# Kernel tuning notes

Hardware: AMD Instinct MI355X
Metric: run time of the kernel (lower is better)

## Reference

```python
import jax, jax.numpy as jnp
import numpy as np

N = 100000   # nodes
E = 1600000  # edges
IN = 32      # in_dim
D = 64       # embed_dim
G = 128      # num graphs
EPS = 1e-5   # BatchNorm eps


def setup_inputs() -> dict:
    key = jax.random.key(0)
    ks = jax.random.split(key, 12)
    s_in = 1.0 / np.sqrt(IN)
    s_d = 1.0 / np.sqrt(D)
    return {
        "x": jax.random.normal(ks[0], (N, IN), jnp.float32),
        "edge_index": jax.random.randint(ks[1], (2, E), 0, N),
        "batch": jnp.sort(jax.random.randint(ks[2], (N,), 0, G)),
        "W_embed": jax.random.normal(ks[3], (IN, D), jnp.float32) * s_in,
        "W1": jax.random.normal(ks[4], (D, D), jnp.float32) * s_d,
        "b1": jnp.zeros((D,), jnp.float32),
        "g1": jnp.ones((D,), jnp.float32),
        "bt1": jnp.zeros((D,), jnp.float32),
        "W2": jax.random.normal(ks[5], (D, D), jnp.float32) * s_d,
        "b2": jnp.zeros((D,), jnp.float32),
        "g2": jnp.ones((D,), jnp.float32),
        "bt2": jnp.zeros((D,), jnp.float32),
    }


def reference(x, edge_index, batch, W_embed, W1, b1, g1, bt1, W2, b2, g2, bt2):
    src, dst = edge_index[0], edge_index[1]
    # GCN symmetric norm with self loops: deg = in-degree + 1 (self loop)
    deg = jnp.zeros((N,), x.dtype).at[dst].add(1.0) + 1.0
    dis = jax.lax.rsqrt(deg)                      # deg^{-1/2}, [N]
    enorm = dis[src] * dis[dst]                   # per-edge norm, [E]
    self_norm = dis * dis                         # self-loop norm, [N]

    def gcn_bn(h, W, b, g, bt, relu):
        hw = h @ W                                # linear first (GCNConv)
        msg = hw[src] * enorm[:, None]            # [E, D] gather + scale
        agg = jax.ops.segment_sum(msg, dst, num_segments=N)
        agg = agg + hw * self_norm[:, None] + b   # self loops + bias
        # BatchNorm1d (training mode: batch stats, biased var)
        mu = agg.mean(axis=0)
        var = agg.var(axis=0)
        hn = (agg - mu) * jax.lax.rsqrt(var + EPS) * g + bt
        return jnp.maximum(hn, 0.0) if relu else hn

    h = x @ W_embed                               # node_embed (Linear, no bias)
    h = gcn_bn(h, W1, b1, g1, bt1, relu=True)     # ReLU only between layers
    h = gcn_bn(h, W2, b2, g2, bt2, relu=False)
    h_pool = jax.ops.segment_sum(h, batch, num_segments=G)  # global_add_pool
    return (h, h_pool)
```

## Files before the change

kernel.cpp:

```cpp
#include <hip/hip_runtime.h>

#define NN 100000
#define NE 1600000
#define IN_DIM 32
#define DD 64
#define NG 128
#define BN_EPS 1e-5f
#define AGG_BLOCKS 2048

typedef unsigned short ushort_t;
typedef unsigned int uint_t;

__device__ __forceinline__ ushort_t f2bf(float f) {
    uint_t u = __float_as_uint(f);
    u = (u + 0x7FFFu + ((u >> 16) & 1u)) >> 16;
    return (ushort_t)u;
}
__device__ __forceinline__ uint_t pack2(float a, float b) {
    return (uint_t)f2bf(a) | ((uint_t)f2bf(b) << 16);
}
__device__ __forceinline__ float bflo(uint_t u) { return __uint_as_float(u << 16); }
__device__ __forceinline__ float bfhi(uint_t u) { return __uint_as_float(u & 0xFFFF0000u); }

__global__ void init_k(int* __restrict__ ints, long n_ints, float* __restrict__ pool,
                       float* __restrict__ sums) {
    long i = (long)blockIdx.x * blockDim.x + threadIdx.x;
    if (i < n_ints) ints[i] = 0;
    if (i < (long)NG * DD) pool[i] = 0.f;
    if (i < 256) sums[i] = 0.f;
}

__global__ void deg_count(const int* __restrict__ dst, int* __restrict__ cnt) {
    int e = blockIdx.x * blockDim.x + threadIdx.x;
    if (e < NE) atomicAdd(&cnt[dst[e]], 1);
}

__global__ __launch_bounds__(256) void alloc_k(const int* __restrict__ cnt,
                                               int* __restrict__ start,
                                               int* __restrict__ cursor,
                                               float* __restrict__ dis) {
    __shared__ int ls[256];
    __shared__ int base_s;
    int t = threadIdx.x;
    long n = (long)blockIdx.x * 256 + t;
    int v = (n < NN) ? cnt[n] : 0;
    ls[t] = v;
    __syncthreads();
    for (int off = 1; off < 256; off <<= 1) {
        int y = (t >= off) ? ls[t - off] : 0;
        __syncthreads();
        ls[t] += y;
        __syncthreads();
    }
    if (t == 0) base_s = atomicAdd(cursor, ls[255]);
    __syncthreads();
    if (n < NN) {
        start[n] = base_s + ls[t] - v;
        dis[n] = rsqrtf((float)v + 1.0f);
    }
}

__global__ void fill_edges(const int* __restrict__ src, const int* __restrict__ dstp,
                           const float* __restrict__ dis, const int* __restrict__ start,
                           int* __restrict__ cur, uint_t* __restrict__ ep) {
    int e = blockIdx.x * blockDim.x + threadIdx.x;
    if (e >= NE) return;
    int s = src[e], t = dstp[e];
    int p = atomicAdd(&cur[t], 1);
    float nm = dis[s] * dis[t];
    uint_t nb = (__float_as_uint(nm) + 0x8000u) >> 16;
    ep[start[t] + p] = (uint_t)s | ((nb & 0x7FFFu) << 17);
}

__global__ __launch_bounds__(256) void mm1_k(const float* __restrict__ x,
                                             const float* __restrict__ We,
                                             const float* __restrict__ W1,
                                             ushort_t* __restrict__ hwb) {
    __shared__ float W1s[DD * DD];
    __shared__ float Ws[IN_DIM * DD];
    int t = threadIdx.x;
    for (int i = t; i < DD * DD; i += 256) W1s[i] = W1[i];
    __syncthreads();
    for (int idx = t; idx < IN_DIM * DD; idx += 256) {
        int i = idx >> 6, j = idx & 63;
        float s = 0.f;
#pragma unroll
        for (int k = 0; k < DD; ++k) s += We[i * DD + k] * W1s[k * DD + j];
        Ws[idx] = s;
    }
    __syncthreads();
    long n = (long)blockIdx.x * 256 + t;
    if (n >= NN) return;
    float acc[DD];
#pragma unroll
    for (int d = 0; d < DD; ++d) acc[d] = 0.f;
    const float4* xr = (const float4*)(x + n * IN_DIM);
#pragma unroll
    for (int k4 = 0; k4 < IN_DIM / 4; ++k4) {
        float4 xv = xr[k4];
        const float* xp = (const float*)&xv;
#pragma unroll
        for (int kk = 0; kk < 4; ++kk) {
            float v = xp[kk];
            int k = k4 * 4 + kk;
#pragma unroll
            for (int d = 0; d < DD; ++d) acc[d] += v * Ws[k * DD + d];
        }
    }
    uint4* o = (uint4*)(hwb + n * DD);
#pragma unroll
    for (int d8 = 0; d8 < DD / 8; ++d8) {
        uint4 pk;
        pk.x = pack2(acc[8 * d8 + 0], acc[8 * d8 + 1]);
        pk.y = pack2(acc[8 * d8 + 2], acc[8 * d8 + 3]);
        pk.z = pack2(acc[8 * d8 + 4], acc[8 * d8 + 5]);
        pk.w = pack2(acc[8 * d8 + 6], acc[8 * d8 + 7]);
        o[d8] = pk;
    }
}

__global__ __launch_bounds__(256) void mm2_bn_k(const ushort_t* __restrict__ aggb,
                                                const float* __restrict__ sums,
                                                const float* __restrict__ g,
                                                const float* __restrict__ bt,
                                                const float* __restrict__ W,
                                                ushort_t* __restrict__ hwb) {
    __shared__ float Ws[DD * DD];
    __shared__ float mu_s[DD], sc_s[DD], bt_s[DD];
    int t = threadIdx.x;
    for (int i = t; i < DD * DD; i += 256) Ws[i] = W[i];
    if (t < DD) {
        const float inv_n = 1.0f / (float)NN;
        float mu = sums[t] * inv_n;
        float var = sums[64 + t] * inv_n - mu * mu;
        mu_s[t] = mu;
        sc_s[t] = g[t] * rsqrtf(var + BN_EPS);
        bt_s[t] = bt[t];
    }
    __syncthreads();
    long n = (long)blockIdx.x * 256 + t;
    if (n >= NN) return;
    float acc[DD];
#pragma unroll
    for (int d = 0; d < DD; ++d) acc[d] = 0.f;
    const uint4* ar = (const uint4*)(aggb + n * DD);
#pragma unroll
    for (int k8 = 0; k8 < DD / 8; ++k8) {
        uint4 av = ar[k8];
        float hv[8];
        hv[0] = bflo(av.x); hv[1] = bfhi(av.x);
        hv[2] = bflo(av.y); hv[3] = bfhi(av.y);
        hv[4] = bflo(av.z); hv[5] = bfhi(av.z);
        hv[6] = bflo(av.w); hv[7] = bfhi(av.w);
#pragma unroll
        for (int kk = 0; kk < 8; ++kk) {
            int k = k8 * 8 + kk;
            float h = fmaxf((hv[kk] - mu_s[k]) * sc_s[k] + bt_s[k], 0.f);
#pragma unroll
            for (int d = 0; d < DD; ++d) acc[d] += h * Ws[k * DD + d];
        }
    }
    uint4* o = (uint4*)(hwb + n * DD);
#pragma unroll
    for (int d8 = 0; d8 < DD / 8; ++d8) {
        uint4 pk;
        pk.x = pack2(acc[8 * d8 + 0], acc[8 * d8 + 1]);
        pk.y = pack2(acc[8 * d8 + 2], acc[8 * d8 + 3]);
        pk.z = pack2(acc[8 * d8 + 4], acc[8 * d8 + 5]);
        pk.w = pack2(acc[8 * d8 + 6], acc[8 * d8 + 7]);
        o[d8] = pk;
    }
}

template <int WAGG_BF16>
__global__ __launch_bounds__(256) void gcn_agg(const ushort_t* __restrict__ hwb,
                                               const float* __restrict__ dis,
                                               const int* __restrict__ cnt,
                                               const int* __restrict__ start,
                                               const uint_t* __restrict__ ep,
                                               const float* __restrict__ bias,
                                               void* __restrict__ aggv,
                                               float* __restrict__ sums) {
    int t = threadIdx.x;
    int w = t >> 6;
    int lane = t & 63;
    int j = lane >> 3;
    int c = lane & 7;
    float selfmask = (j == 0) ? 1.f : 0.f;

    __shared__ float ls[4][128];
    for (int k = t; k < 512; k += 256) ((float*)ls)[k] = 0.f;
    __syncthreads();

    float bs[8];
#pragma unroll
    for (int k = 0; k < 8; ++k) bs[k] = bias[8 * c + k];

    for (long n = (long)blockIdx.x * 4 + w; n < NN; n += (long)gridDim.x * 4) {
        int rs = start[n];
        int ce = cnt[n];
        float sn = dis[n];
        float sq = sn * sn;

        uint4 sv = ((const uint4*)(hwb + (long)n * DD))[c];
        float acc[8];
        acc[0] = selfmask * (bflo(sv.x) * sq + bs[0]);
        acc[1] = selfmask * (bfhi(sv.x) * sq + bs[1]);
        acc[2] = selfmask * (bflo(sv.y) * sq + bs[2]);
        acc[3] = selfmask * (bfhi(sv.y) * sq + bs[3]);
        acc[4] = selfmask * (bflo(sv.z) * sq + bs[4]);
        acc[5] = selfmask * (bfhi(sv.z) * sq + bs[5]);
        acc[6] = selfmask * (bflo(sv.w) * sq + bs[6]);
        acc[7] = selfmask * (bfhi(sv.w) * sq + bs[7]);

        for (int i = 0; i < ce; i += 32) {
            int i0 = i + j, i1 = i + 8 + j, i2 = i + 16 + j, i3 = i + 24 + j;
            uint_t u0 = (i0 < ce) ? ep[rs + i0] : 0u;
            uint_t u1 = (i1 < ce) ? ep[rs + i1] : 0u;
            uint_t u2 = (i2 < ce) ? ep[rs + i2] : 0u;
            uint_t u3 = (i3 < ce) ? ep[rs + i3] : 0u;
            uint4 q0 = ((const uint4*)(hwb + (long)(u0 & 0x1FFFF) * DD))[c];
            uint4 q1 = ((const uint4*)(hwb + (long)(u1 & 0x1FFFF) * DD))[c];
            uint4 q2 = ((const uint4*)(hwb + (long)(u2 & 0x1FFFF) * DD))[c];
            uint4 q3 = ((const uint4*)(hwb + (long)(u3 & 0x1FFFF) * DD))[c];
            float n0 = __uint_as_float((u0 >> 17) << 16);
            float n1 = __uint_as_float((u1 >> 17) << 16);
            float n2 = __uint_as_float((u2 >> 17) << 16);
            float n3 = __uint_as_float((u3 >> 17) << 16);
            acc[0] += bflo(q0.x) * n0; acc[1] += bfhi(q0.x) * n0;
            acc[2] += bflo(q0.y) * n0; acc[3] += bfhi(q0.y) * n0;
            acc[4] += bflo(q0.z) * n0; acc[5] += bfhi(q0.z) * n0;
            acc[6] += bflo(q0.w) * n0; acc[7] += bfhi(q0.w) * n0;
            acc[0] += bflo(q1.x) * n1; acc[1] += bfhi(q1.x) * n1;
            acc[2] += bflo(q1.y) * n1; acc[3] += bfhi(q1.y) * n1;
            acc[4] += bflo(q1.z) * n1; acc[5] += bfhi(q1.z) * n1;
            acc[6] += bflo(q1.w) * n1; acc[7] += bfhi(q1.w) * n1;
            acc[0] += bflo(q2.x) * n2; acc[1] += bfhi(q2.x) * n2;
            acc[2] += bflo(q2.y) * n2; acc[3] += bfhi(q2.y) * n2;
            acc[4] += bflo(q2.z) * n2; acc[5] += bfhi(q2.z) * n2;
            acc[6] += bflo(q2.w) * n2; acc[7] += bfhi(q2.w) * n2;
            acc[0] += bflo(q3.x) * n3; acc[1] += bfhi(q3.x) * n3;
            acc[2] += bflo(q3.y) * n3; acc[3] += bfhi(q3.y) * n3;
            acc[4] += bflo(q3.z) * n3; acc[5] += bfhi(q3.z) * n3;
            acc[6] += bflo(q3.w) * n3; acc[7] += bfhi(q3.w) * n3;
        }

#pragma unroll
        for (int m = 8; m < 64; m <<= 1) {
#pragma unroll
            for (int k = 0; k < 8; ++k) acc[k] += __shfl_xor(acc[k], m, 64);
        }

        if (j == 0) {
            if (WAGG_BF16) {
                uint4 pk;
                pk.x = pack2(acc[0], acc[1]);
                pk.y = pack2(acc[2], acc[3]);
                pk.z = pack2(acc[4], acc[5]);
                pk.w = pack2(acc[6], acc[7]);
                ((uint4*)((ushort_t*)aggv + (long)n * DD))[c] = pk;
            } else {
                float4* op = (float4*)((float*)aggv + (long)n * DD + 8 * c);
                op[0] = make_float4(acc[0], acc[1], acc[2], acc[3]);
                op[1] = make_float4(acc[4], acc[5], acc[6], acc[7]);
            }
#pragma unroll
            for (int k = 0; k < 8; ++k) {
                ls[w][8 * c + k] += acc[k];
                ls[w][64 + 8 * c + k] += acc[k] * acc[k];
            }
        }
    }

    __syncthreads();
    if (t < 128) {
        float a = ls[0][t] + ls[1][t] + ls[2][t] + ls[3][t];
        atomicAdd(&sums[t], a);
    }
}

__global__ __launch_bounds__(256) void bn_pool(const float* __restrict__ agg,
                                               const float* __restrict__ sums,
                                               const float* __restrict__ g,
                                               const float* __restrict__ bt,
                                               const int* __restrict__ batch,
                                               float* __restrict__ out,
                                               float* __restrict__ pool) {
    int t = threadIdx.x;
    int d = t & 63, rq = t >> 6;
    const float inv_n = 1.0f / (float)NN;
    float mu = sums[d] * inv_n;
    float var = sums[64 + d] * inv_n - mu * mu;
    float sc = g[d] * rsqrtf(var + BN_EPS);
    float bd = bt[d];
    long base = (long)blockIdx.x * 256;
    float acc = 0.f;
    int cur = -1;
    for (int i = 0; i < 64; ++i) {
        long r = base + rq + 4 * i;
        if (r >= NN) break;
        int b = batch[r];
        float v = (agg[r * DD + d] - mu) * sc + bd;
        out[r * DD + d] = v;
        if (b != cur) {
            if (cur >= 0) atomicAdd(&pool[(long)cur * DD + d], acc);
            acc = 0.f;
            cur = b;
        }
        acc += v;
    }
    if (cur >= 0) atomicAdd(&pool[(long)cur * DD + d], acc);
}

extern "C" void kernel_launch(void* const* d_in, const int* in_sizes, int n_in,
                              void* d_out, int out_size, void* d_ws, size_t ws_size,
                              hipStream_t stream) {
    const float* x = (const float*)d_in[0];
    const int* ei = (const int*)d_in[1];
    const int* batch = (const int*)d_in[2];
    const float* W_embed = (const float*)d_in[3];
    const float* W1 = (const float*)d_in[4];
    const float* b1 = (const float*)d_in[5];
    const float* g1 = (const float*)d_in[6];
    const float* bt1 = (const float*)d_in[7];
    const float* W2 = (const float*)d_in[8];
    const float* b2 = (const float*)d_in[9];
    const float* g2 = (const float*)d_in[10];
    const float* bt2 = (const float*)d_in[11];

    const int* src = ei;
    const int* dst = ei + NE;

    float* out = (float*)d_out;
    float* pool = out + (long)NN * DD;

    const long ND = (long)NN * DD;

    char* w = (char*)d_ws;
    int* cnt = (int*)w;           w += sizeof(int) * NN;
    int* cur = (int*)w;           w += sizeof(int) * NN;
    int* cursor = (int*)w;        w += sizeof(int) * 4;
    int* start = (int*)w;         w += sizeof(int) * NN;
    float* dis = (float*)w;       w += sizeof(float) * NN;
    float* sums1 = (float*)w;     w += sizeof(float) * 128;
    float* sums2 = (float*)w;     w += sizeof(float) * 128;
    uint_t* ep = (uint_t*)w;      w += sizeof(uint_t) * NE;
    ushort_t* hwb = (ushort_t*)w; w += sizeof(ushort_t) * ND;
    ushort_t* agg1b = (ushort_t*)w; w += sizeof(ushort_t) * ND;
    float* aggbuf = (float*)w;

    dim3 blk(256);
    const int nbN = (NN + 255) / 256;
    const int nbE = (NE + 255) / 256;
    const long n_ints = 2L * NN + 4;

    init_k<<<dim3((int)((n_ints + 255) / 256)), blk, 0, stream>>>(cnt, n_ints, pool, sums1);
    deg_count<<<dim3(nbE), blk, 0, stream>>>(dst, cnt);
    alloc_k<<<dim3(nbN), blk, 0, stream>>>(cnt, start, cursor, dis);
    fill_edges<<<dim3(nbE), blk, 0, stream>>>(src, dst, dis, start, cur, ep);

    mm1_k<<<dim3(nbN), blk, 0, stream>>>(x, W_embed, W1, hwb);

    gcn_agg<1><<<dim3(AGG_BLOCKS), blk, 0, stream>>>(hwb, dis, cnt, start, ep, b1,
                                                     (void*)agg1b, sums1);

    mm2_bn_k<<<dim3(nbN), blk, 0, stream>>>(agg1b, sums1, g1, bt1, W2, hwb);

    gcn_agg<0><<<dim3(AGG_BLOCKS), blk, 0, stream>>>(hwb, dis, cnt, start, ep, b2,
                                                     (void*)aggbuf, sums2);

    bn_pool<<<dim3(nbN), blk, 0, stream>>>(aggbuf, sums2, g2, bt2, batch, out, pool);
}
```

Measured before the change: 480.1 us.

## Partition degree count and edge fill by destination range; vectorize shared weight reads

Degree counting and CSR edge filling now use 8 destination partitions. Blocks are interleaved across partitions, and each block scans every edge but only performs atomics and writes for destinations in its partition. This aims to keep atomic and scattered write traffic local to one slice of the node arrays, improving cache or XCD locality, at the cost of reading dst eight times. The mm1 and mm2 inner loops also read the shared-memory weights as float4 to cut LDS instruction count.

```diff
diff --git a/kernel.cpp b/kernel.cpp
--- a/kernel.cpp
+++ b/kernel.cpp
@@ -7,6 +7,9 @@
 #define NG 128
 #define BN_EPS 1e-5f
 #define AGG_BLOCKS 2048
+#define NPART 8
+#define PSZ ((NN + NPART - 1) / NPART)
+#define PBLK 64
 
 typedef unsigned short ushort_t;
 typedef unsigned int uint_t;
@@ -30,9 +33,17 @@
     if (i < 256) sums[i] = 0.f;
 }
 
-__global__ void deg_count(const int* __restrict__ dst, int* __restrict__ cnt) {
-    int e = blockIdx.x * blockDim.x + threadIdx.x;
-    if (e < NE) atomicAdd(&cnt[dst[e]], 1);
+__global__ __launch_bounds__(256) void deg_count_p(const int* __restrict__ dst,
+                                                   int* __restrict__ cnt) {
+    int part = blockIdx.x & 7;
+    int bi = blockIdx.x >> 3;
+    int lo = part * PSZ;
+    int hi = (lo + PSZ < NN) ? lo + PSZ : NN;
+    const long stride = (long)PBLK * 256;
+    for (long e = (long)bi * 256 + threadIdx.x; e < NE; e += stride) {
+        int t = dst[e];
+        if (t >= lo && t < hi) atomicAdd(&cnt[t], 1);
+    }
 }
 
 __global__ __launch_bounds__(256) void alloc_k(const int* __restrict__ cnt,
@@ -60,16 +71,27 @@
     }
 }
 
-__global__ void fill_edges(const int* __restrict__ src, const int* __restrict__ dstp,
-                           const float* __restrict__ dis, const int* __restrict__ start,
-                           int* __restrict__ cur, uint_t* __restrict__ ep) {
-    int e = blockIdx.x * blockDim.x + threadIdx.x;
-    if (e >= NE) return;
-    int s = src[e], t = dstp[e];
-    int p = atomicAdd(&cur[t], 1);
-    float nm = dis[s] * dis[t];
-    uint_t nb = (__float_as_uint(nm) + 0x8000u) >> 16;
-    ep[start[t] + p] = (uint_t)s | ((nb & 0x7FFFu) << 17);
+__global__ __launch_bounds__(256) void fill_edges_p(const int* __restrict__ src,
+                                                    const int* __restrict__ dstp,
+                                                    const float* __restrict__ dis,
+                                                    const int* __restrict__ start,
+                                                    int* __restrict__ cur,
+                                                    uint_t* __restrict__ ep) {
+    int part = blockIdx.x & 7;
+    int bi = blockIdx.x >> 3;
+    int lo = part * PSZ;
+    int hi = (lo + PSZ < NN) ? lo + PSZ : NN;
+    const long stride = (long)PBLK * 256;
+    for (long e = (long)bi * 256 + threadIdx.x; e < NE; e += stride) {
+        int t = dstp[e];
+        if (t >= lo && t < hi) {
+            int s = src[e];
+            int p = atomicAdd(&cur[t], 1);
+            float nm = dis[s] * dis[t];
+            uint_t nb = (__float_as_uint(nm) + 0x8000u) >> 16;
+            ep[start[t] + p] = (uint_t)s | ((nb & 0x7FFFu) << 17);
+        }
+    }
 }
 
 __global__ __launch_bounds__(256) void mm1_k(const float* __restrict__ x,
@@ -102,9 +124,15 @@
 #pragma unroll
         for (int kk = 0; kk < 4; ++kk) {
             float v = xp[kk];
-            int k = k4 * 4 + kk;
-#pragma unroll
-            for (int d = 0; d < DD; ++d) acc[d] += v * Ws[k * DD + d];
+            const float4* w4 = (const float4*)&Ws[(k4 * 4 + kk) * DD];
+#pragma unroll
+            for (int d4 = 0; d4 < DD / 4; ++d4) {
+                float4 wv = w4[d4];
+                acc[4 * d4 + 0] += v * wv.x;
+                acc[4 * d4 + 1] += v * wv.y;
+                acc[4 * d4 + 2] += v * wv.z;
+                acc[4 * d4 + 3] += v * wv.w;
+            }
         }
     }
     uint4* o = (uint4*)(hwb + n * DD);
@@ -156,8 +184,15 @@
         for (int kk = 0; kk < 8; ++kk) {
             int k = k8 * 8 + kk;
             float h = fmaxf((hv[kk] - mu_s[k]) * sc_s[k] + bt_s[k], 0.f);
-#pragma unroll
-            for (int d = 0; d < DD; ++d) acc[d] += h * Ws[k * DD + d];
+            const float4* w4 = (const float4*)&Ws[k * DD];
+#pragma unroll
+            for (int d4 = 0; d4 < DD / 4; ++d4) {
+                float4 wv = w4[d4];
+                acc[4 * d4 + 0] += h * wv.x;
+                acc[4 * d4 + 1] += h * wv.y;
+                acc[4 * d4 + 2] += h * wv.z;
+                acc[4 * d4 + 3] += h * wv.w;
+            }
         }
     }
     uint4* o = (uint4*)(hwb + n * DD);
@@ -351,13 +386,12 @@
 
     dim3 blk(256);
     const int nbN = (NN + 255) / 256;
-    const int nbE = (NE + 255) / 256;
     const long n_ints = 2L * NN + 4;
 
     init_k<<<dim3((int)((n_ints + 255) / 256)), blk, 0, stream>>>(cnt, n_ints, pool, sums1);
-    deg_count<<<dim3(nbE), blk, 0, stream>>>(dst, cnt);
+    deg_count_p<<<dim3(NPART * PBLK), blk, 0, stream>>>(dst, cnt);
     alloc_k<<<dim3(nbN), blk, 0, stream>>>(cnt, start, cursor, dis);
-    fill_edges<<<dim3(nbE), blk, 0, stream>>>(src, dst, dis, start, cur, ep);
+    fill_edges_p<<<dim3(NPART * PBLK), blk, 0, stream>>>(src, dst, dis, start, cur, ep);
 
     mm1_k<<<dim3(nbN), blk, 0, stream>>>(x, W_embed, W1, hwb);
 
```

Measured after the change: 494.2 us. +2.9%, slower.
